# Kernel tuning notes

Measured on AMD Instinct MI355X. Metric: run time of the kernel, lower is better.

The kernel has to match this reference:

```python
import jax, jax.numpy as jnp
import numpy as np

H = 256  # hidden_size
B = 8192  # batch
S = 1024  # seq_length


def setup_inputs() -> dict:
    key = jax.random.key(0)
    ks = jax.random.split(key, 12)
    lim_g = 1.0 / np.sqrt(1 + H)  # torch Linear default init bound, fan_in = 1+H
    lim_o = 1.0 / np.sqrt(H)
    def lin(k, out_dim, in_dim, lim):
        kw, kb = jax.random.split(k)
        W = jax.random.uniform(kw, (out_dim, in_dim), jnp.float32, -lim, lim)
        b = jax.random.uniform(kb, (out_dim,), jnp.float32, -lim, lim)
        return W, b
    Wf, bf = lin(ks[0], H, 1 + H, lim_g)
    Wi, bi = lin(ks[1], H, 1 + H, lim_g)
    Wc, bc = lin(ks[2], H, 1 + H, lim_g)
    Wo, bo = lin(ks[3], H, 1 + H, lim_g)
    Wout, bout = lin(ks[4], 1, H, lim_o)
    x = jax.random.normal(ks[5], (B, S), jnp.float32)
    return {"x": x, "Wf": Wf, "bf": bf, "Wi": Wi, "bi": bi,
            "Wc": Wc, "bc": bc, "Wo": Wo, "bo": bo,
            "Wout": Wout, "bout": bout}


def reference(x, Wf, bf, Wi, bi, Wc, bc, Wo, bo, Wout, bout):
    B_, S_ = x.shape
    H_ = Wf.shape[0]
    # Fuse the four gate linears into one GEMM per step (same math):
    Wall = jnp.concatenate([Wf, Wi, Wc, Wo], axis=0)      # [4H, 1+H]
    ball = jnp.concatenate([bf, bi, bc, bo], axis=0)      # [4H]

    def step(carry, xt):
        h, c = carry                                       # [B,H], [B,H]
        conc = jnp.concatenate([xt[:, None], h], axis=1)   # [B, 1+H]
        g = conc @ Wall.T + ball                           # [B, 4H]
        f, i, cs, o = jnp.split(g, 4, axis=1)
        c = jax.nn.sigmoid(f) * c + jax.nn.sigmoid(i) * jnp.tanh(cs)
        h = jax.nn.sigmoid(o) * jnp.tanh(c)
        return (h, c), None

    h0 = jnp.zeros((B_, H_), x.dtype)
    c0 = jnp.zeros((B_, H_), x.dtype)
    (h, _), _ = jax.lax.scan(step, (h0, c0), x.T)          # scan over seq axis
    out = h @ Wout.T + bout                                # [B, 1]
    return out.squeeze(-1)                                 # [B]
```

## Files before the change

### kernel.cpp

```cpp
#include <hip/hip_runtime.h>
#include <hip/hip_fp16.h>


typedef _Float16 f16x8 __attribute__((ext_vector_type(8)));
typedef float f32x4 __attribute__((ext_vector_type(4)));
typedef unsigned int u32;
typedef unsigned short u16;

#define WINT_OFF 0u
#define W0B_OFF  524288u
#define FLAG_OFF 528384u
#define PUB_OFF  1048576u

static __device__ __forceinline__ float fast_exp2(float x) {
#if __has_builtin(__builtin_amdgcn_exp2f)
  return __builtin_amdgcn_exp2f(x);
#else
  return exp2f(x);
#endif
}
static __device__ __forceinline__ float fast_rcp(float x) {
#if __has_builtin(__builtin_amdgcn_rcpf)
  return __builtin_amdgcn_rcpf(x);
#else
  return 1.0f / x;
#endif
}
static __device__ __forceinline__ u16 f16b(float f) {
  union { _Float16 h; u16 u; } cv; cv.h = (_Float16)f; return cv.u;
}
static __device__ __forceinline__ float h2f(u16 u) {
  union { u16 u; _Float16 h; } cv; cv.u = u; return (float)cv.h;
}
static __device__ __forceinline__ u16* pub_base(u16* pub, int set, int par,
                                                int pid, int half) {
  return pub + ((size_t)(((set * 2 + par) * 128 + pid) * 2 + half) << 12);
}

__global__ void lstm_prep(const float* __restrict__ Wf, const float* __restrict__ Wi,
                          const float* __restrict__ Wc, const float* __restrict__ Wo,
                          const float* __restrict__ bf_, const float* __restrict__ bi_,
                          const float* __restrict__ bc_, const float* __restrict__ bo_,
                          u16* __restrict__ Wint, u32* __restrict__ w0b) {
  int n = blockIdx.x;
  int k = threadIdx.x;
  int g = n >> 8, j = n & 255;
  const float* Ws = (g == 0) ? Wf : (g == 1) ? Wi : (g == 2) ? Wc : Wo;
  const float scale = (g == 2) ? 2.88539008f : 1.44269504f;
  Wint[n * 256 + k] = f16b(Ws[j * 257 + 1 + k] * scale);
  if (k == 0) {
    const float* bs = (g == 0) ? bf_ : (g == 1) ? bi_ : (g == 2) ? bc_ : bo_;
    w0b[n] = (u32)f16b(Ws[j * 257] * scale) | ((u32)f16b(bs[j] * scale) << 16);
  }
}

__global__ void lstm_zero(uint4* __restrict__ pub4, uint4* __restrict__ flags4,
                          float* __restrict__ out, const float* __restrict__ bout) {
  int idx = blockIdx.x * 256 + threadIdx.x;
  uint4 z = uint4{0, 0, 0, 0};
  if (idx < 131072) pub4[idx] = z;
  else if (idx < 262144) pub4[idx + 131072] = z;
  else if (idx < 264192) flags4[idx - 262144] = z;
  else { int o = idx - 264192; if (o < 8192) out[o] = bout[0]; }
}

__global__ __launch_bounds__(512, 2) void lstm_main(
    const u16* __restrict__ Wint, const u32* __restrict__ w0b,
    const float* __restrict__ x, const float* __restrict__ Wout,
    float* __restrict__ out, u16* __restrict__ pub, int* __restrict__ flags) {

  __shared__ __align__(16) u16 stg[2][2][2][4096];

  const int tid  = threadIdx.x;
  const int wv   = tid >> 6;
  const int lane = tid & 63;
  const int l15  = lane & 15;
  const int quad = lane >> 4;
  const int grp  = (wv & 1) ^ ((wv >> 2) & 1);
  const int B    = blockIdx.x;
  const int mi   = (B >> 3) & 1;
  const int peer = B ^ 8;
  const int pid  = (B & 7) | ((B >> 4) << 3);
  const int rows0 = pid * 64;

  f16x8 wfrag[4][8];
#pragma unroll
  for (int g = 0; g < 4; ++g)
#pragma unroll
    for (int hm = 0; hm < 2; ++hm)
#pragma unroll
      for (int ktl = 0; ktl < 4; ++ktl) {
        int kbase = (hm == 0 ? mi : 1 - mi) * 128 + ktl * 32;
        wfrag[g][hm * 4 + ktl] = *(const f16x8*)(Wint +
            (size_t)(g * 256 + mi * 128 + wv * 16 + l15) * 256 + kbase + quad * 8);
      }
  float w0f[4][4], bsf[4][4];
#pragma unroll
  for (int g = 0; g < 4; ++g) {
    uint4 wv4 = *(const uint4*)(w0b + g * 256 + mi * 128 + wv * 16 + quad * 4);
    u32 pka[4] = {wv4.x, wv4.y, wv4.z, wv4.w};
#pragma unroll
    for (int r = 0; r < 4; ++r) {
      w0f[g][r] = h2f((u16)pka[r]);
      bsf[g][r] = h2f((u16)(pka[r] >> 16));
    }
  }

#pragma unroll
  for (int i = 0; i < 8; ++i) ((uint4*)stg)[tid + i * 512] = uint4{0, 0, 0, 0};

  float cst[2][2][4];
#pragma unroll
  for (int s = 0; s < 2; ++s)
#pragma unroll
    for (int bt = 0; bt < 2; ++bt)
#pragma unroll
      for (int r = 0; r < 4; ++r) cst[s][bt][r] = 0.0f;

  f32x4 acc[4][2];

  const float* xq = x + (size_t)rows0 * 1024;
  float xcur[2][2];
#pragma unroll
  for (int s = 0; s < 2; ++s)
#pragma unroll
    for (int bt = 0; bt < 2; ++bt)
      xcur[s][bt] = xq[(size_t)(s * 32 + bt * 16 + l15) * 1024];

  int* const myflag = flags + B * 32;
  int* const pfl    = flags + peer * 32;

  __syncthreads();

#define DO_K(S, T, LEAD) do {                                                  \
    const int par_ = (T) & 1;                                                  \
    if (LEAD) {                                                                \
      while (__hip_atomic_load(pfl + (S) * 16, __ATOMIC_RELAXED,               \
                               __HIP_MEMORY_SCOPE_AGENT) < (T))                \
        __builtin_amdgcn_s_sleep(1);                                           \
      const u16* srcP_ = pub_base(pub, (S), par_, pid, 1 - mi);                \
      u16* dst_ = &stg[S][par_][1][0];                                         \
      _Pragma("unroll")                                                        \
      for (int i_ = 0; i_ < 8; ++i_)                                           \
        __builtin_amdgcn_global_load_lds(                                      \
            (const __attribute__((address_space(1))) u32*)(srcP_ + i_ * 512 + lane * 8), \
            (__attribute__((address_space(3))) u32*)(dst_ + i_ * 512), 16, 0, 0); \
      __builtin_amdgcn_sched_barrier(0);                                       \
    }                                                                          \
    _Pragma("unroll")                                                          \
    for (int g_ = 0; g_ < 4; ++g_)                                             \
      _Pragma("unroll")                                                        \
      for (int r_ = 0; r_ < 4; ++r_) {                                         \
        acc[g_][0][r_] = xcur[S][0] * w0f[g_][r_] + bsf[g_][r_];               \
        acc[g_][1][r_] = xcur[S][1] * w0f[g_][r_] + bsf[g_][r_];               \
      }                                                                        \
    _Pragma("unroll")                                                          \
    for (int ktl_ = 0; ktl_ < 4; ++ktl_) {                                     \
      f16x8 bb_[2];                                                            \
      _Pragma("unroll")                                                        \
      for (int bt_ = 0; bt_ < 2; ++bt_) {                                      \
        int b_ = bt_ * 16 + l15;                                               \
        int cp_ = (ktl_ * 4 + quad) ^ (b_ & 15);                               \
        bb_[bt_] = *(const f16x8*)(&stg[S][par_][0][0] + b_ * 128 + cp_ * 8);  \
      }                                                                        \
      _Pragma("unroll")                                                        \
      for (int g_ = 0; g_ < 4; ++g_)                                           \
        _Pragma("unroll")                                                      \
        for (int bt_ = 0; bt_ < 2; ++bt_)                                      \
          acc[g_][bt_] = __builtin_amdgcn_mfma_f32_16x16x32_f16(               \
              wfrag[g_][ktl_], bb_[bt_], acc[g_][bt_], 0, 0, 0);               \
    }                                                                          \
    if (LEAD) {                                                                \
      asm volatile("s_waitcnt vmcnt(0)" ::: "memory");                         \
      __builtin_amdgcn_sched_barrier(0);                                       \
    }                                                                          \
    _Pragma("unroll")                                                          \
    for (int ktl_ = 0; ktl_ < 4; ++ktl_) {                                     \
      f16x8 bb_[2];                                                            \
      _Pragma("unroll")                                                        \
      for (int bt_ = 0; bt_ < 2; ++bt_) {                                      \
        int b_ = bt_ * 16 + l15;                                               \
        int cp_ = (ktl_ * 4 + quad) ^ (b_ & 15);                               \
        bb_[bt_] = *(const f16x8*)(&stg[S][par_][1][0] + b_ * 128 + cp_ * 8);  \
      }                                                                        \
      _Pragma("unroll")                                                        \
      for (int g_ = 0; g_ < 4; ++g_)                                           \
        _Pragma("unroll")                                                      \
        for (int bt_ = 0; bt_ < 2; ++bt_)                                      \
          acc[g_][bt_] = __builtin_amdgcn_mfma_f32_16x16x32_f16(               \
              wfrag[g_][4 + ktl_], bb_[bt_], acc[g_][bt_], 0, 0, 0);           \
    }                                                                          \
  } while (0)

#define DO_EW(S, TEW) do {                                                     \
    const int parn_ = ((TEW) + 1) & 1;                                         \
    u16* pb_ = pub_base(pub, (S), parn_, pid, mi);                             \
    u16* lb_ = &stg[S][parn_][0][0];                                           \
    _Pragma("unroll")                                                          \
    for (int bt_ = 0; bt_ < 2; ++bt_) {                                        \
      int b_ = bt_ * 16 + l15;                                                 \
      u32 lo_, hi_;                                                            \
      {                                                                        \
        float h0_, h1_, h2_, h3_;                                              \
        _Pragma("unroll")                                                      \
        for (int r_ = 0; r_ < 4; ++r_) {                                       \
          float fg_ = acc[0][bt_][r_], ig_ = acc[1][bt_][r_];                  \
          float cg_ = acc[2][bt_][r_], og_ = acc[3][bt_][r_];                  \
          float Ef_ = fast_exp2(-fg_);                                         \
          float Ei_ = fast_exp2(-ig_);                                         \
          float C_  = fast_exp2(cg_);                                          \
          float X_  = 1.0f + Ef_;                                              \
          float Y_  = (1.0f + Ei_) * (C_ + 1.0f);                              \
          float num_ = cst[S][bt_][r_] * Y_ + (C_ - 1.0f) * X_;                \
          float c2_  = num_ * fast_rcp(X_ * Y_);                               \
          cst[S][bt_][r_] = c2_;                                               \
          float cc_ = fminf(fmaxf(c2_, -40.0f), 40.0f);                        \
          float T_  = fast_exp2(2.88539008f * cc_);                            \
          float Eo_ = fast_exp2(-og_);                                         \
          float hv_ = (T_ - 1.0f) * fast_rcp((1.0f + Eo_) * (T_ + 1.0f));      \
          if (r_ == 0) h0_ = hv_; else if (r_ == 1) h1_ = hv_;                 \
          else if (r_ == 2) h2_ = hv_; else h3_ = hv_;                         \
        }                                                                      \
        lo_ = (u32)f16b(h0_) | ((u32)f16b(h1_) << 16);                         \
        hi_ = (u32)f16b(h2_) | ((u32)f16b(h3_) << 16);                         \
      }                                                                        \
      int c16_ = wv * 2 + (quad >> 1);                                         \
      int off_ = b_ * 128 + (c16_ ^ (b_ & 15)) * 8 + (quad & 1) * 4;           \
      *(uint2*)(lb_ + off_) = uint2{lo_, hi_};                                 \
      *(uint2*)(pb_ + off_) = uint2{lo_, hi_};                                 \
    }                                                                          \
  } while (0)

#pragma unroll 1
  for (int t = 0; t < 1024; ++t) {
    if (grp == 0) {
      DO_K(0, t, 1);
    } else {
      if (t > 0) DO_EW(1, t - 1);
      xcur[1][0] = xq[(size_t)(32 + l15) * 1024 + t];
      xcur[1][1] = xq[(size_t)(48 + l15) * 1024 + t];
    }
    __syncthreads();
    if (tid == 0)
      __hip_atomic_store(myflag + 16, t, __ATOMIC_RELAXED,
                         __HIP_MEMORY_SCOPE_AGENT);

    if (grp == 0) DO_EW(0, t);
    else          DO_K(0, t, 0);
    __syncthreads();

    if (grp == 0) {
      DO_K(1, t, 1);
    } else {
      DO_EW(0, t);
      xcur[0][0] = xq[(size_t)(l15) * 1024 + ((t + 1) & 1023)];
      xcur[0][1] = xq[(size_t)(16 + l15) * 1024 + ((t + 1) & 1023)];
    }
    __syncthreads();
    if (tid == 0)
      __hip_atomic_store(myflag + 0, t + 1, __ATOMIC_RELAXED,
                         __HIP_MEMORY_SCOPE_AGENT);

    if (grp == 0) {
      DO_EW(1, t);
      xcur[0][0] = xq[(size_t)(l15) * 1024 + ((t + 1) & 1023)];
      xcur[0][1] = xq[(size_t)(16 + l15) * 1024 + ((t + 1) & 1023)];
      xcur[1][0] = xq[(size_t)(32 + l15) * 1024 + ((t + 1) & 1023)];
      xcur[1][1] = xq[(size_t)(48 + l15) * 1024 + ((t + 1) & 1023)];
    } else {
      DO_K(1, t, 0);
    }
    __syncthreads();
  }

  if (grp == 1) DO_EW(1, 1023);
  __syncthreads();

  if (tid < 64) {
    int s = tid >> 5, b = tid & 31;
    const u16* pbase = pub_base(pub, s, 0, pid, mi);
    float a = 0.0f;
#pragma unroll
    for (int c = 0; c < 16; ++c) {
      f16x8 hv = *(const f16x8*)(pbase + b * 128 + ((c ^ (b & 15)) * 8));
#pragma unroll
      for (int e = 0; e < 8; ++e) a += (float)hv[e] * Wout[mi * 128 + c * 8 + e];
    }
    atomicAdd(&out[rows0 + s * 32 + b], a);
  }
#undef DO_K
#undef DO_EW
}

extern "C" void kernel_launch(void* const* d_in, const int* in_sizes, int n_in,
                              void* d_out, int out_size, void* d_ws, size_t ws_size,
                              hipStream_t stream) {
  const float* x    = (const float*)d_in[0];
  const float* Wf   = (const float*)d_in[1];
  const float* bf_  = (const float*)d_in[2];
  const float* Wi   = (const float*)d_in[3];
  const float* bi_  = (const float*)d_in[4];
  const float* Wc   = (const float*)d_in[5];
  const float* bc_  = (const float*)d_in[6];
  const float* Wo   = (const float*)d_in[7];
  const float* bo_  = (const float*)d_in[8];
  const float* Wout = (const float*)d_in[9];
  const float* bout = (const float*)d_in[10];

  u16* Wint  = (u16*)((char*)d_ws + WINT_OFF);
  u32* w0b   = (u32*)((char*)d_ws + W0B_OFF);
  int* flags = (int*)((char*)d_ws + FLAG_OFF);
  u16* pub   = (u16*)((char*)d_ws + PUB_OFF);

  lstm_prep<<<1024, 256, 0, stream>>>(Wf, Wi, Wc, Wo, bf_, bi_, bc_, bo_, Wint, w0b);
  lstm_zero<<<1064, 256, 0, stream>>>((uint4*)pub, (uint4*)flags, (float*)d_out, bout);
  lstm_main<<<256, 512, 0, stream>>>(Wint, w0b, x, Wout, (float*)d_out, pub, flags);
}
```

Before: 5.439 ms.

## Replace wave-group ping-pong with uniform per-block two-stream software pipeline

Removes the split of waves into compute and elementwise groups; all waves now run both matmul and gate elementwise work, interleaving the two independent batch streams so one stream's elementwise step overlaps the other's local-half MFMAs before waiting on the peer block. LDS staging drops its parity double buffer, accumulators are kept per stream, and bias/x-weight constants are unpacked on the fly to save registers. The zero kernel no longer clears the publish buffer, since a peeled first step writes it before it is read. This risks races from the single-buffered LDS and published data, and adds register pressure from the doubled accumulators.

```diff
diff --git a/kernel.cpp b/kernel.cpp
--- a/kernel.cpp
+++ b/kernel.cpp
@@ -54,14 +54,11 @@
   }
 }
 
-__global__ void lstm_zero(uint4* __restrict__ pub4, uint4* __restrict__ flags4,
-                          float* __restrict__ out, const float* __restrict__ bout) {
+__global__ void lstm_zero(uint4* __restrict__ flags4, float* __restrict__ out,
+                          const float* __restrict__ bout) {
   int idx = blockIdx.x * 256 + threadIdx.x;
-  uint4 z = uint4{0, 0, 0, 0};
-  if (idx < 131072) pub4[idx] = z;
-  else if (idx < 262144) pub4[idx + 131072] = z;
-  else if (idx < 264192) flags4[idx - 262144] = z;
-  else { int o = idx - 264192; if (o < 8192) out[o] = bout[0]; }
+  if (idx < 2048) flags4[idx] = uint4{0, 0, 0, 0};
+  else if (idx < 10240) out[idx - 2048] = bout[0];
 }
 
 __global__ __launch_bounds__(512, 2) void lstm_main(
@@ -69,14 +66,13 @@
     const float* __restrict__ x, const float* __restrict__ Wout,
     float* __restrict__ out, u16* __restrict__ pub, int* __restrict__ flags) {
 
-  __shared__ __align__(16) u16 stg[2][2][2][4096];
+  __shared__ __align__(16) u16 stg[2][2][4096];
 
   const int tid  = threadIdx.x;
   const int wv   = tid >> 6;
   const int lane = tid & 63;
   const int l15  = lane & 15;
   const int quad = lane >> 4;
-  const int grp  = (wv & 1) ^ ((wv >> 2) & 1);
   const int B    = blockIdx.x;
   const int mi   = (B >> 3) & 1;
   const int peer = B ^ 8;
@@ -94,20 +90,13 @@
         wfrag[g][hm * 4 + ktl] = *(const f16x8*)(Wint +
             (size_t)(g * 256 + mi * 128 + wv * 16 + l15) * 256 + kbase + quad * 8);
       }
-  float w0f[4][4], bsf[4][4];
-#pragma unroll
-  for (int g = 0; g < 4; ++g) {
-    uint4 wv4 = *(const uint4*)(w0b + g * 256 + mi * 128 + wv * 16 + quad * 4);
-    u32 pka[4] = {wv4.x, wv4.y, wv4.z, wv4.w};
-#pragma unroll
-    for (int r = 0; r < 4; ++r) {
-      w0f[g][r] = h2f((u16)pka[r]);
-      bsf[g][r] = h2f((u16)(pka[r] >> 16));
-    }
-  }
-
-#pragma unroll
-  for (int i = 0; i < 8; ++i) ((uint4*)stg)[tid + i * 512] = uint4{0, 0, 0, 0};
+  uint4 w0bv[4];
+#pragma unroll
+  for (int g = 0; g < 4; ++g)
+    w0bv[g] = *(const uint4*)(w0b + g * 256 + mi * 128 + wv * 16 + quad * 4);
+
+#pragma unroll
+  for (int i = 0; i < 4; ++i) ((uint4*)stg)[tid + i * 512] = uint4{0, 0, 0, 0};
 
   float cst[2][2][4];
 #pragma unroll
@@ -117,7 +106,7 @@
 #pragma unroll
       for (int r = 0; r < 4; ++r) cst[s][bt][r] = 0.0f;
 
-  f32x4 acc[4][2];
+  f32x4 acc[2][4][2];
 
   const float* xq = x + (size_t)rows0 * 1024;
   float xcur[2][2];
@@ -132,70 +121,25 @@
 
   __syncthreads();
 
-#define DO_K(S, T, LEAD) do {                                                  \
-    const int par_ = (T) & 1;                                                  \
-    if (LEAD) {                                                                \
-      while (__hip_atomic_load(pfl + (S) * 16, __ATOMIC_RELAXED,               \
-                               __HIP_MEMORY_SCOPE_AGENT) < (T))                \
-        __builtin_amdgcn_s_sleep(1);                                           \
-      const u16* srcP_ = pub_base(pub, (S), par_, pid, 1 - mi);                \
-      u16* dst_ = &stg[S][par_][1][0];                                         \
-      _Pragma("unroll")                                                        \
-      for (int i_ = 0; i_ < 8; ++i_)                                           \
-        __builtin_amdgcn_global_load_lds(                                      \
-            (const __attribute__((address_space(1))) u32*)(srcP_ + i_ * 512 + lane * 8), \
-            (__attribute__((address_space(3))) u32*)(dst_ + i_ * 512), 16, 0, 0); \
-      __builtin_amdgcn_sched_barrier(0);                                       \
-    }                                                                          \
-    _Pragma("unroll")                                                          \
-    for (int g_ = 0; g_ < 4; ++g_)                                             \
+#define ACC_INIT(S) do {                                                       \
+    _Pragma("unroll")                                                          \
+    for (int g_ = 0; g_ < 4; ++g_) {                                           \
+      u32 pka_[4] = {w0bv[g_].x, w0bv[g_].y, w0bv[g_].z, w0bv[g_].w};          \
       _Pragma("unroll")                                                        \
       for (int r_ = 0; r_ < 4; ++r_) {                                         \
-        acc[g_][0][r_] = xcur[S][0] * w0f[g_][r_] + bsf[g_][r_];               \
-        acc[g_][1][r_] = xcur[S][1] * w0f[g_][r_] + bsf[g_][r_];               \
+        float w0_ = h2f((u16)pka_[r_]), bs_ = h2f((u16)(pka_[r_] >> 16));      \
+        acc[S][g_][0][r_] = xcur[S][0] * w0_ + bs_;                            \
+        acc[S][g_][1][r_] = xcur[S][1] * w0_ + bs_;                            \
       }                                                                        \
-    _Pragma("unroll")                                                          \
-    for (int ktl_ = 0; ktl_ < 4; ++ktl_) {                                     \
-      f16x8 bb_[2];                                                            \
-      _Pragma("unroll")                                                        \
-      for (int bt_ = 0; bt_ < 2; ++bt_) {                                      \
-        int b_ = bt_ * 16 + l15;                                               \
-        int cp_ = (ktl_ * 4 + quad) ^ (b_ & 15);                               \
-        bb_[bt_] = *(const f16x8*)(&stg[S][par_][0][0] + b_ * 128 + cp_ * 8);  \
-      }                                                                        \
-      _Pragma("unroll")                                                        \
-      for (int g_ = 0; g_ < 4; ++g_)                                           \
-        _Pragma("unroll")                                                      \
-        for (int bt_ = 0; bt_ < 2; ++bt_)                                      \
-          acc[g_][bt_] = __builtin_amdgcn_mfma_f32_16x16x32_f16(               \
-              wfrag[g_][ktl_], bb_[bt_], acc[g_][bt_], 0, 0, 0);               \
     }                                                                          \
-    if (LEAD) {                                                                \
-      asm volatile("s_waitcnt vmcnt(0)" ::: "memory");                         \
-      __builtin_amdgcn_sched_barrier(0);                                       \
-    }                                                                          \
-    _Pragma("unroll")                                                          \
-    for (int ktl_ = 0; ktl_ < 4; ++ktl_) {                                     \
-      f16x8 bb_[2];                                                            \
-      _Pragma("unroll")                                                        \
-      for (int bt_ = 0; bt_ < 2; ++bt_) {                                      \
-        int b_ = bt_ * 16 + l15;                                               \
-        int cp_ = (ktl_ * 4 + quad) ^ (b_ & 15);                               \
-        bb_[bt_] = *(const f16x8*)(&stg[S][par_][1][0] + b_ * 128 + cp_ * 8);  \
-      }                                                                        \
-      _Pragma("unroll")                                                        \
-      for (int g_ = 0; g_ < 4; ++g_)                                           \
-        _Pragma("unroll")                                                      \
-        for (int bt_ = 0; bt_ < 2; ++bt_)                                      \
-          acc[g_][bt_] = __builtin_amdgcn_mfma_f32_16x16x32_f16(               \
-              wfrag[g_][4 + ktl_], bb_[bt_], acc[g_][bt_], 0, 0, 0);           \
-    }                                                                          \
-  } while (0)
-
-#define DO_EW(S, TEW) do {                                                     \
-    const int parn_ = ((TEW) + 1) & 1;                                         \
-    u16* pb_ = pub_base(pub, (S), parn_, pid, mi);                             \
-    u16* lb_ = &stg[S][parn_][0][0];                                           \
+    _Pragma("unroll")                                                          \
+    for (int bt_ = 0; bt_ < 2; ++bt_)                                          \
+      xcur[S][bt_] = xq[(size_t)((S) * 32 + bt_ * 16 + l15) * 1024 +           \
+                        ((t + 1) & 1023)];                                     \
+  } while (0)
+
+#define EW_PUB(ES, TP1) do {                                                   \
+    u16* pb_ = pub_base(pub, ES, (TP1) & 1, pid, mi);                          \
     _Pragma("unroll")                                                          \
     for (int bt_ = 0; bt_ < 2; ++bt_) {                                        \
       int b_ = bt_ * 16 + l15;                                                 \
@@ -204,16 +148,16 @@
         float h0_, h1_, h2_, h3_;                                              \
         _Pragma("unroll")                                                      \
         for (int r_ = 0; r_ < 4; ++r_) {                                       \
-          float fg_ = acc[0][bt_][r_], ig_ = acc[1][bt_][r_];                  \
-          float cg_ = acc[2][bt_][r_], og_ = acc[3][bt_][r_];                  \
+          float fg_ = acc[ES][0][bt_][r_], ig_ = acc[ES][1][bt_][r_];          \
+          float cg_ = acc[ES][2][bt_][r_], og_ = acc[ES][3][bt_][r_];          \
           float Ef_ = fast_exp2(-fg_);                                         \
           float Ei_ = fast_exp2(-ig_);                                         \
           float C_  = fast_exp2(cg_);                                          \
           float X_  = 1.0f + Ef_;                                              \
           float Y_  = (1.0f + Ei_) * (C_ + 1.0f);                              \
-          float num_ = cst[S][bt_][r_] * Y_ + (C_ - 1.0f) * X_;                \
+          float num_ = cst[ES][bt_][r_] * Y_ + (C_ - 1.0f) * X_;               \
           float c2_  = num_ * fast_rcp(X_ * Y_);                               \
-          cst[S][bt_][r_] = c2_;                                               \
+          cst[ES][bt_][r_] = c2_;                                              \
           float cc_ = fminf(fmaxf(c2_, -40.0f), 40.0f);                        \
           float T_  = fast_exp2(2.88539008f * cc_);                            \
           float Eo_ = fast_exp2(-og_);                                         \
@@ -226,54 +170,87 @@
       }                                                                        \
       int c16_ = wv * 2 + (quad >> 1);                                         \
       int off_ = b_ * 128 + (c16_ ^ (b_ & 15)) * 8 + (quad & 1) * 4;           \
-      *(uint2*)(lb_ + off_) = uint2{lo_, hi_};                                 \
+      *(uint2*)(&stg[ES][0][0] + off_) = uint2{lo_, hi_};                      \
       *(uint2*)(pb_ + off_) = uint2{lo_, hi_};                                 \
     }                                                                          \
   } while (0)
 
+#define KHALF(S, HM) do {                                                      \
+    _Pragma("unroll")                                                          \
+    for (int ktl_ = 0; ktl_ < 4; ++ktl_) {                                     \
+      f16x8 bb_[2];                                                            \
+      _Pragma("unroll")                                                        \
+      for (int bt_ = 0; bt_ < 2; ++bt_) {                                      \
+        int b_ = bt_ * 16 + l15;                                               \
+        int cp_ = (ktl_ * 4 + quad) ^ (b_ & 15);                               \
+        bb_[bt_] = *(const f16x8*)(&stg[S][HM][0] + b_ * 128 + cp_ * 8);       \
+      }                                                                        \
+      _Pragma("unroll")                                                        \
+      for (int g_ = 0; g_ < 4; ++g_)                                           \
+        _Pragma("unroll")                                                      \
+        for (int bt_ = 0; bt_ < 2; ++bt_)                                      \
+          acc[S][g_][bt_] = __builtin_amdgcn_mfma_f32_16x16x32_f16(            \
+              wfrag[g_][(HM) * 4 + ktl_], bb_[bt_], acc[S][g_][bt_], 0, 0, 0); \
+    }                                                                          \
+  } while (0)
+
+#define DMA_PEER_FULL(S, T) do {                                               \
+    const u16* srcP_ = pub_base(pub, S, (T) & 1, pid, 1 - mi);                 \
+    _Pragma("unroll")                                                          \
+    for (int i_ = 0; i_ < 8; ++i_)                                             \
+      __builtin_amdgcn_global_load_lds(                                        \
+          (const __attribute__((address_space(1))) u32*)(srcP_ + i_ * 512 +    \
+                                                         lane * 8),            \
+          (__attribute__((address_space(3))) u32*)(&stg[S][1][i_ * 512]),      \
+          16, 0, 0);                                                           \
+  } while (0)
+
+  {
+    const int t = 0;
+    ACC_INIT(0);
+    KHALF(0, 0); KHALF(0, 1);
+    __syncthreads();
+    ACC_INIT(1);
+    EW_PUB(0, 1);
+    KHALF(1, 0); KHALF(1, 1);
+    __syncthreads();
+    if (tid == 0)
+      __hip_atomic_store(myflag + 0, 1, __ATOMIC_RELAXED,
+                         __HIP_MEMORY_SCOPE_AGENT);
+  }
+
 #pragma unroll 1
-  for (int t = 0; t < 1024; ++t) {
-    if (grp == 0) {
-      DO_K(0, t, 1);
-    } else {
-      if (t > 0) DO_EW(1, t - 1);
-      xcur[1][0] = xq[(size_t)(32 + l15) * 1024 + t];
-      xcur[1][1] = xq[(size_t)(48 + l15) * 1024 + t];
-    }
+  for (int t = 1; t < 1024; ++t) {
+    ACC_INIT(0);
+    EW_PUB(1, t);
+    KHALF(0, 0);
+    while (__hip_atomic_load(pfl + 0, __ATOMIC_RELAXED,
+                             __HIP_MEMORY_SCOPE_AGENT) < t)
+      __builtin_amdgcn_s_sleep(1);
+    DMA_PEER_FULL(0, t);
+    asm volatile("s_waitcnt vmcnt(0)" ::: "memory");
+    KHALF(0, 1);
     __syncthreads();
     if (tid == 0)
       __hip_atomic_store(myflag + 16, t, __ATOMIC_RELAXED,
                          __HIP_MEMORY_SCOPE_AGENT);
 
-    if (grp == 0) DO_EW(0, t);
-    else          DO_K(0, t, 0);
-    __syncthreads();
-
-    if (grp == 0) {
-      DO_K(1, t, 1);
-    } else {
-      DO_EW(0, t);
-      xcur[0][0] = xq[(size_t)(l15) * 1024 + ((t + 1) & 1023)];
-      xcur[0][1] = xq[(size_t)(16 + l15) * 1024 + ((t + 1) & 1023)];
-    }
+    ACC_INIT(1);
+    EW_PUB(0, t + 1);
+    KHALF(1, 0);
+    while (__hip_atomic_load(pfl + 16, __ATOMIC_RELAXED,
+                             __HIP_MEMORY_SCOPE_AGENT) < t)
+      __builtin_amdgcn_s_sleep(1);
+    DMA_PEER_FULL(1, t);
+    asm volatile("s_waitcnt vmcnt(0)" ::: "memory");
+    KHALF(1, 1);
     __syncthreads();
     if (tid == 0)
       __hip_atomic_store(myflag + 0, t + 1, __ATOMIC_RELAXED,
                          __HIP_MEMORY_SCOPE_AGENT);
-
-    if (grp == 0) {
-      DO_EW(1, t);
-      xcur[0][0] = xq[(size_t)(l15) * 1024 + ((t + 1) & 1023)];
-      xcur[0][1] = xq[(size_t)(16 + l15) * 1024 + ((t + 1) & 1023)];
-      xcur[1][0] = xq[(size_t)(32 + l15) * 1024 + ((t + 1) & 1023)];
-      xcur[1][1] = xq[(size_t)(48 + l15) * 1024 + ((t + 1) & 1023)];
-    } else {
-      DO_K(1, t, 0);
-    }
-    __syncthreads();
-  }
-
-  if (grp == 1) DO_EW(1, 1023);
+  }
+
+  EW_PUB(1, 1024);
   __syncthreads();
 
   if (tid < 64) {
@@ -288,8 +265,10 @@
     }
     atomicAdd(&out[rows0 + s * 32 + b], a);
   }
-#undef DO_K
-#undef DO_EW
+#undef ACC_INIT
+#undef EW_PUB
+#undef KHALF
+#undef DMA_PEER_FULL
 }
 
 extern "C" void kernel_launch(void* const* d_in, const int* in_sizes, int n_in,
@@ -313,6 +292,6 @@
   u16* pub   = (u16*)((char*)d_ws + PUB_OFF);
 
   lstm_prep<<<1024, 256, 0, stream>>>(Wf, Wi, Wc, Wo, bf_, bi_, bc_, bo_, Wint, w0b);
-  lstm_zero<<<1064, 256, 0, stream>>>((uint4*)pub, (uint4*)flags, (float*)d_out, bout);
+  lstm_zero<<<40, 256, 0, stream>>>((uint4*)flags, (float*)d_out, bout);
   lstm_main<<<256, 512, 0, stream>>>(Wint, w0b, x, Wout, (float*)d_out, pub, flags);
 }
```

After: 6.580 ms. 21.0% more time.
